# Optimization experiments

Measured on AMD Instinct MI355X. Metric: run time of the kernel, lower is better.

Reference implementation:

```python
import jax, jax.numpy as jnp
import numpy as np

B, L, D, H = 64, 1024, 256, 256


def setup_inputs() -> dict:
    key = jax.random.key(0)
    ks = jax.random.split(key, 10)
    s = 0.05  # small init to keep tanh/sigmoid in linear-ish range
    return {
        "x":  jax.random.normal(ks[0], (B, L, D), jnp.float32),
        # LSTM cell params (keras gate order i, f, g, o)
        "Wk": jax.random.normal(ks[1], (D, 4 * H), jnp.float32) * s,
        "Wr": jax.random.normal(ks[2], (H, 4 * H), jnp.float32) * s,
        "b":  jnp.zeros((4 * H,), jnp.float32),
        # Attention params
        "W1": jax.random.normal(ks[3], (D, H), jnp.float32) * s,
        "b1": jnp.zeros((H,), jnp.float32),
        "W2": jax.random.normal(ks[4], (H, H), jnp.float32) * s,
        "b2": jnp.zeros((H,), jnp.float32),
        "V":  jax.random.normal(ks[5], (H, 1), jnp.float32) * s,
        "bV": jnp.zeros((1,), jnp.float32),
    }


def reference(x, Wk, Wr, b, W1, b1, W2, b2, V, bV):
    Bb, Ll, Dd = x.shape
    Hh = Wr.shape[0]
    # Encoder projection, computed once (W1 @ encoder_outputs)
    w1_e = jnp.einsum('bld,dh->blh', x, W1) + b1            # (B, L, H)
    # Decoder input is the last encoder step, repeated every step
    x_in = x[:, -1, :]                                      # (B, D)
    xz = x_in @ Wk + b                                      # (B, 4H), constant per step
    h0 = jnp.zeros((Bb, Hh), x.dtype)
    c0 = jnp.zeros((Bb, Hh), x.dtype)

    def step(carry, _):
        h, c = carry
        z = xz + h @ Wr                                     # (B, 4H)
        i, f, g, o = jnp.split(z, 4, axis=-1)
        i = jax.nn.sigmoid(i)
        f = jax.nn.sigmoid(f)
        g = jnp.tanh(g)
        o = jax.nn.sigmoid(o)
        c = f * c + i * g
        h = o * jnp.tanh(c)
        # Additive (Bahdanau) attention: v^T tanh(W1 e + W2 d)
        w2_d = (h @ W2 + b2)[:, None, :]                    # (B, 1, H)
        scores = jnp.tanh(w1_e + w2_d) @ V + bV             # (B, L, 1)
        attn = jax.nn.softmax(scores[..., 0], axis=1)       # (B, L)
        return (h, c), attn

    _, attn_seq = jax.lax.scan(step, (h0, c0), None, length=Ll)  # (L, B, L)
    return jnp.transpose(attn_seq, (1, 0, 2))               # (B, L_steps, L_ptr)
```

## Files before the change

kernel.cpp:

```cpp
#include <hip/hip_runtime.h>
#include <hip/hip_bf16.h>


#define LOG2E  1.4426950408889634f
#define C2LOG2E 2.8853900817779268f

__device__ __forceinline__ unsigned f2bf(float f) {
  unsigned u = __builtin_bit_cast(unsigned, f);
  return (u + 0x7fffu + ((u >> 16) & 1u)) >> 16;
}
__device__ __forceinline__ float bfbits2f(unsigned bits) {
  return __builtin_bit_cast(float, bits << 16);
}

#if defined(__has_builtin)
#  if __has_builtin(__builtin_amdgcn_fdot2_f32_bf16)
#    define HAS_DOT2_BF16 1
#  endif
#endif

#if defined(HAS_DOT2_BF16)
typedef __bf16 bf16x2v __attribute__((ext_vector_type(2)));
__device__ __forceinline__ float dot2bf(unsigned w, unsigned h, float acc) {
  return __builtin_amdgcn_fdot2_f32_bf16(__builtin_bit_cast(bf16x2v, w),
                                         __builtin_bit_cast(bf16x2v, h), acc, false);
}
#else
__device__ __forceinline__ float dot2bf(unsigned w, unsigned h, float acc) {
  float wl = __builtin_bit_cast(float, w << 16);
  float wh = __builtin_bit_cast(float, w & 0xffff0000u);
  float hl = __builtin_bit_cast(float, h << 16);
  float hh = __builtin_bit_cast(float, h & 0xffff0000u);
  return fmaf(wh, hh, fmaf(wl, hl, acc));
}
#endif

#if defined(__has_builtin) && __has_builtin(__builtin_amdgcn_rcpf)
#  define FAST_RCP(x) __builtin_amdgcn_rcpf(x)
#else
#  define FAST_RCP(x) (1.0f / (x))
#endif

__device__ __forceinline__ float fast_sigmoid(float x) {
  return FAST_RCP(1.f + exp2f(-LOG2E * x));
}
__device__ __forceinline__ float fast_tanh(float x) {
  return 1.f - 2.f * FAST_RCP(1.f + exp2f(C2LOG2E * x));
}

__global__ __launch_bounds__(256) void k1_w1e(const float* __restrict__ x,
                                              const float* __restrict__ W1,
                                              const float* __restrict__ b1,
                                              unsigned short* __restrict__ AT) {
  const int b  = blockIdx.x >> 6;
  const int lb = blockIdx.x & 63;
  const int h  = threadIdx.x;
  float acc[16];
  const float bias = b1[h];
#pragma unroll
  for (int r = 0; r < 16; ++r) acc[r] = bias;
  const float* xb = x + ((size_t)(b * 1024 + lb * 16)) * 256;
  for (int d0 = 0; d0 < 256; d0 += 4) {
    const float w0 = W1[(d0 + 0) * 256 + h];
    const float w1 = W1[(d0 + 1) * 256 + h];
    const float w2 = W1[(d0 + 2) * 256 + h];
    const float w3 = W1[(d0 + 3) * 256 + h];
#pragma unroll
    for (int r = 0; r < 16; ++r) {
      const float4 xv = *(const float4*)(xb + r * 256 + d0);
      acc[r] = fmaf(xv.x, w0, acc[r]);
      acc[r] = fmaf(xv.y, w1, acc[r]);
      acc[r] = fmaf(xv.z, w2, acc[r]);
      acc[r] = fmaf(xv.w, w3, acc[r]);
    }
  }
  unsigned short* outp = AT + ((size_t)(b * 256 + h)) * 1024 + lb * 16;
#pragma unroll
  for (int r = 0; r < 16; r += 2) {
    unsigned u0 = f2bf(exp2f(C2LOG2E * acc[r]));
    unsigned u1 = f2bf(exp2f(C2LOG2E * acc[r + 1]));
    *(unsigned*)(outp + r) = u0 | (u1 << 16);
  }
}

__global__ __launch_bounds__(256) void k2_xz(const float* __restrict__ x,
                                             const float* __restrict__ Wk,
                                             const float* __restrict__ bvec,
                                             float* __restrict__ xz) {
  const int b = blockIdx.x, tid = threadIdx.x;
  float acc[4] = {bvec[tid], bvec[256 + tid], bvec[512 + tid], bvec[768 + tid]};
  const float* xr = x + ((size_t)b * 1024 + 1023) * 256;
  for (int d0 = 0; d0 < 256; d0 += 4) {
    const float4 xv = *(const float4*)(xr + d0);
#pragma unroll
    for (int i = 0; i < 4; ++i) {
      const float xs = (i == 0) ? xv.x : (i == 1) ? xv.y : (i == 2) ? xv.z : xv.w;
#pragma unroll
      for (int q = 0; q < 4; ++q)
        acc[q] = fmaf(xs, Wk[(size_t)(d0 + i) * 1024 + q * 256 + tid], acc[q]);
    }
  }
#pragma unroll
  for (int q = 0; q < 4; ++q) xz[b * 1024 + q * 256 + tid] = acc[q];
}

__global__ __launch_bounds__(512, 2) void k3_recur(const float* __restrict__ xz,
                                                   const float* __restrict__ Wr,
                                                   unsigned short* __restrict__ hseq) {
  __shared__ __align__(16) unsigned Wtail[8 * 1024 * 4];
  __shared__ float z_lds[512];
  __shared__ __align__(16) unsigned h_pk[128];
  const int b   = blockIdx.x;
  const int tid = threadIdx.x;
  const int colA = tid, colB = tid + 512;

  unsigned wA[96], wB[96];
#pragma unroll
  for (int p = 0; p < 96; ++p) {
    wA[p] = f2bf(Wr[(size_t)(2 * p) * 1024 + colA]) |
            (f2bf(Wr[(size_t)(2 * p + 1) * 1024 + colA]) << 16);
    wB[p] = f2bf(Wr[(size_t)(2 * p) * 1024 + colB]) |
            (f2bf(Wr[(size_t)(2 * p + 1) * 1024 + colB]) << 16);
  }
#pragma unroll
  for (int gg = 0; gg < 8; ++gg) {
#pragma unroll
    for (int d = 0; d < 4; ++d) {
      const int p = 96 + gg * 4 + d;
      Wtail[(gg * 1024 + colA) * 4 + d] =
          f2bf(Wr[(size_t)(2 * p) * 1024 + colA]) |
          (f2bf(Wr[(size_t)(2 * p + 1) * 1024 + colA]) << 16);
      Wtail[(gg * 1024 + colB) * 4 + d] =
          f2bf(Wr[(size_t)(2 * p) * 1024 + colB]) |
          (f2bf(Wr[(size_t)(2 * p + 1) * 1024 + colB]) << 16);
    }
  }
  if (tid < 128) h_pk[tid] = 0u;
  const float zaA = xz[b * 1024 + colA];
  const float zaB = xz[b * 1024 + colB];
  float c = 0.f;
  __syncthreads();

  for (int t = 0; t < 1024; ++t) {
    float aA = zaA, aB = zaB;
#pragma unroll
    for (int g = 0; g < 24; ++g) {
      const uint4 hp = *(const uint4*)&h_pk[4 * g];
      aA = dot2bf(wA[4 * g + 0], hp.x, aA);
      aA = dot2bf(wA[4 * g + 1], hp.y, aA);
      aA = dot2bf(wA[4 * g + 2], hp.z, aA);
      aA = dot2bf(wA[4 * g + 3], hp.w, aA);
      aB = dot2bf(wB[4 * g + 0], hp.x, aB);
      aB = dot2bf(wB[4 * g + 1], hp.y, aB);
      aB = dot2bf(wB[4 * g + 2], hp.z, aB);
      aB = dot2bf(wB[4 * g + 3], hp.w, aB);
    }
#pragma unroll
    for (int gg = 0; gg < 8; ++gg) {
      const uint4 hp = *(const uint4*)&h_pk[96 + 4 * gg];
      const uint4 wa = *(const uint4*)&Wtail[(gg * 1024 + colA) * 4];
      const uint4 wb = *(const uint4*)&Wtail[(gg * 1024 + colB) * 4];
      aA = dot2bf(wa.x, hp.x, aA);
      aA = dot2bf(wa.y, hp.y, aA);
      aA = dot2bf(wa.z, hp.z, aA);
      aA = dot2bf(wa.w, hp.w, aA);
      aB = dot2bf(wb.x, hp.x, aB);
      aB = dot2bf(wb.y, hp.y, aB);
      aB = dot2bf(wb.z, hp.z, aB);
      aB = dot2bf(wb.w, hp.w, aB);
    }
    if (tid >= 256) {
      z_lds[tid - 256] = aA;
      z_lds[tid]       = aB;
    }
    __syncthreads();
    if (tid < 256) {
      const float zi = aA;
      const float zg = aB;
      const float zf = z_lds[tid];
      const float zo = z_lds[tid + 256];
      const float ig = fast_sigmoid(zi);
      const float fg = fast_sigmoid(zf);
      const float gv = fast_tanh(zg);
      const float og = fast_sigmoid(zo);
      c = fmaf(fg, c, ig * gv);
      const float h = og * fast_tanh(c);
      const unsigned short hb = (unsigned short)f2bf(h);
      ((unsigned short*)h_pk)[tid] = hb;
      hseq[(size_t)(t * 64 + b) * 256 + tid] = hb;
    }
    __syncthreads();
  }
}

__global__ __launch_bounds__(256) void k3b_w2d(const unsigned int* __restrict__ hseq,
                                               const float* __restrict__ W2,
                                               const float* __restrict__ b2,
                                               float* __restrict__ D) {
  const int r0 = blockIdx.x * 16;
  const int h = threadIdx.x;
  float acc[16];
  const float bias = b2[h];
#pragma unroll
  for (int r = 0; r < 16; ++r) acc[r] = bias;
  for (int m0 = 0; m0 < 128; m0 += 2) {
    const float w0 = W2[(size_t)(2 * m0 + 0) * 256 + h];
    const float w1 = W2[(size_t)(2 * m0 + 1) * 256 + h];
    const float w2 = W2[(size_t)(2 * m0 + 2) * 256 + h];
    const float w3 = W2[(size_t)(2 * m0 + 3) * 256 + h];
#pragma unroll
    for (int r = 0; r < 16; ++r) {
      const uint2 hp = *(const uint2*)&hseq[(size_t)(r0 + r) * 128 + m0];
      acc[r] = fmaf(bfbits2f(hp.x),       w0, acc[r]);
      acc[r] = fmaf(bfbits2f(hp.x >> 16), w1, acc[r]);
      acc[r] = fmaf(bfbits2f(hp.y),       w2, acc[r]);
      acc[r] = fmaf(bfbits2f(hp.y >> 16), w3, acc[r]);
    }
  }
  const int t = r0 >> 6;
  const int bb0 = r0 & 63;
#pragma unroll
  for (int r = 0; r < 16; ++r) {
    D[((size_t)(bb0 + r) * 1024 + t) * 256 + h] = exp2f(C2LOG2E * acc[r]);
  }
}

__global__ __launch_bounds__(256) void k4_attn(const unsigned short* __restrict__ AT,
                                               const float* __restrict__ Dm,
                                               const float* __restrict__ V,
                                               float* __restrict__ out) {
  const int b  = blockIdx.x >> 6;
  const int tb = blockIdx.x & 63;
  const int wv = threadIdx.x >> 6;
  const int lane = threadIdx.x & 63;
  const int t0 = tb * 16 + wv * 4;
  const unsigned short* Ab = AT + (size_t)b * 256 * 1024;
  const float* Db = Dm + ((size_t)b * 1024 + t0) * 256;
  float acc[4][16];
#pragma unroll
  for (int tt = 0; tt < 4; ++tt)
#pragma unroll
    for (int lb = 0; lb < 16; ++lb) acc[tt][lb] = 0.f;

  for (int h = 0; h < 256; ++h) {
    const float vh = V[h];
    const float d0 = Db[h];
    const float d1 = Db[256 + h];
    const float d2 = Db[512 + h];
    const float d3 = Db[768 + h];
    const unsigned short* Ah = Ab + h * 1024 + lane;
#pragma unroll
    for (int lb = 0; lb < 16; ++lb) {
      const float a = bfbits2f((unsigned)Ah[lb * 64]);
      acc[0][lb] = fmaf(vh, FAST_RCP(fmaf(a, d0, 1.f)), acc[0][lb]);
      acc[1][lb] = fmaf(vh, FAST_RCP(fmaf(a, d1, 1.f)), acc[1][lb]);
      acc[2][lb] = fmaf(vh, FAST_RCP(fmaf(a, d2, 1.f)), acc[2][lb]);
      acc[3][lb] = fmaf(vh, FAST_RCP(fmaf(a, d3, 1.f)), acc[3][lb]);
    }
  }
#pragma unroll
  for (int tt = 0; tt < 4; ++tt) {
    float s[16];
    float m = -1e30f;
#pragma unroll
    for (int lb = 0; lb < 16; ++lb) {
      s[lb] = -2.f * acc[tt][lb];
      m = fmaxf(m, s[lb]);
    }
    for (int off = 32; off > 0; off >>= 1) m = fmaxf(m, __shfl_xor(m, off, 64));
    float p[16];
    float sum = 0.f;
#pragma unroll
    for (int lb = 0; lb < 16; ++lb) {
      p[lb] = exp2f((s[lb] - m) * LOG2E);
      sum += p[lb];
    }
    for (int off = 32; off > 0; off >>= 1) sum += __shfl_xor(sum, off, 64);
    const float rs = 1.f / sum;
    float* op = out + ((size_t)(b * 1024) + (t0 + tt)) * 1024 + lane;
#pragma unroll
    for (int lb = 0; lb < 16; ++lb) op[lb * 64] = p[lb] * rs;
  }
}

extern "C" void kernel_launch(void* const* d_in, const int* in_sizes, int n_in,
                              void* d_out, int out_size, void* d_ws, size_t ws_size,
                              hipStream_t stream) {
  (void)in_sizes; (void)n_in; (void)out_size; (void)ws_size;
  const float* x  = (const float*)d_in[0];
  const float* Wk = (const float*)d_in[1];
  const float* Wr = (const float*)d_in[2];
  const float* bb = (const float*)d_in[3];
  const float* W1 = (const float*)d_in[4];
  const float* b1 = (const float*)d_in[5];
  const float* W2 = (const float*)d_in[6];
  const float* b2 = (const float*)d_in[7];
  const float* V  = (const float*)d_in[8];

  char* ws = (char*)d_ws;
  float*          Dm   = (float*)(ws);
  unsigned short* AT   = (unsigned short*)(ws + 67108864);
  unsigned short* hseq = (unsigned short*)(ws + 100663296);
  float*          xz   = (float*)(ws + 134217728);
  float* out = (float*)d_out;

  hipLaunchKernelGGL(k1_w1e, dim3(4096), dim3(256), 0, stream, x, W1, b1, AT);
  hipLaunchKernelGGL(k2_xz, dim3(64), dim3(256), 0, stream, x, Wk, bb, xz);
  hipLaunchKernelGGL(k3_recur, dim3(64), dim3(512), 0, stream, xz, Wr, hseq);
  hipLaunchKernelGGL(k3b_w2d, dim3(4096), dim3(256), 0, stream, (const unsigned int*)hseq, W2, b2, Dm);
  hipLaunchKernelGGL(k4_attn, dim3(4096), dim3(256), 0, stream, AT, Dm, V, out);
}
```

Before: 4.266 ms.

## Combine four reciprocals into one and pack A in quads for attention

The attention kernel now sums four terms v_h/(1+a*d) over a common denominator, so it needs one fast reciprocal per four h values. It works on pairs of time steps with packed float2 math. To feed this, k1 rearranges the A tensor through shared memory so that four consecutive h values sit together as uint2 per position, letting k4 load them with one 8-byte access. The recurrent kernel also splits each dot-product chain into two accumulators to shorten the dependency chain. The trade is more multiplies and possible overflow or precision loss in the product of four denominators, plus an extra LDS transpose in k1.

```diff
diff --git a/kernel.cpp b/kernel.cpp
--- a/kernel.cpp
+++ b/kernel.cpp
@@ -4,6 +4,8 @@
 
 #define LOG2E  1.4426950408889634f
 #define C2LOG2E 2.8853900817779268f
+
+typedef float f32x2 __attribute__((ext_vector_type(2)));
 
 __device__ __forceinline__ unsigned f2bf(float f) {
   unsigned u = __builtin_bit_cast(unsigned, f);
@@ -11,6 +13,9 @@
 }
 __device__ __forceinline__ float bfbits2f(unsigned bits) {
   return __builtin_bit_cast(float, bits << 16);
+}
+__device__ __forceinline__ float bfhi2f(unsigned bits) {
+  return __builtin_bit_cast(float, bits & 0xffff0000u);
 }
 
 #if defined(__has_builtin)
@@ -51,7 +56,8 @@
 __global__ __launch_bounds__(256) void k1_w1e(const float* __restrict__ x,
                                               const float* __restrict__ W1,
                                               const float* __restrict__ b1,
-                                              unsigned short* __restrict__ AT) {
+                                              uint2* __restrict__ ATq) {
+  __shared__ unsigned short tile[256 * 16];
   const int b  = blockIdx.x >> 6;
   const int lb = blockIdx.x & 63;
   const int h  = threadIdx.x;
@@ -74,12 +80,22 @@
       acc[r] = fmaf(xv.w, w3, acc[r]);
     }
   }
-  unsigned short* outp = AT + ((size_t)(b * 256 + h)) * 1024 + lb * 16;
-#pragma unroll
-  for (int r = 0; r < 16; r += 2) {
-    unsigned u0 = f2bf(exp2f(C2LOG2E * acc[r]));
-    unsigned u1 = f2bf(exp2f(C2LOG2E * acc[r + 1]));
-    *(unsigned*)(outp + r) = u0 | (u1 << 16);
+#pragma unroll
+  for (int r = 0; r < 16; ++r)
+    tile[h * 16 + r] = (unsigned short)f2bf(exp2f(C2LOG2E * acc[r]));
+  __syncthreads();
+#pragma unroll
+  for (int k = 0; k < 4; ++k) {
+    const int o = k * 256 + threadIdx.x;
+    const int hq = o >> 4, lloc = o & 15;
+    const unsigned s0 = tile[(4 * hq + 0) * 16 + lloc];
+    const unsigned s1 = tile[(4 * hq + 1) * 16 + lloc];
+    const unsigned s2 = tile[(4 * hq + 2) * 16 + lloc];
+    const unsigned s3 = tile[(4 * hq + 3) * 16 + lloc];
+    uint2 val;
+    val.x = s0 | (s1 << 16);
+    val.y = s2 | (s3 << 16);
+    ATq[(((size_t)(b * 64 + hq)) << 10) + lb * 16 + lloc] = val;
   }
 }
 
@@ -142,33 +158,49 @@
   __syncthreads();
 
   for (int t = 0; t < 1024; ++t) {
-    float aA = zaA, aB = zaB;
-#pragma unroll
-    for (int g = 0; g < 24; ++g) {
+    float aA0 = zaA, aA1 = 0.f, aB0 = zaB, aB1 = 0.f;
+#pragma unroll
+    for (int g = 0; g < 12; ++g) {
       const uint4 hp = *(const uint4*)&h_pk[4 * g];
-      aA = dot2bf(wA[4 * g + 0], hp.x, aA);
-      aA = dot2bf(wA[4 * g + 1], hp.y, aA);
-      aA = dot2bf(wA[4 * g + 2], hp.z, aA);
-      aA = dot2bf(wA[4 * g + 3], hp.w, aA);
-      aB = dot2bf(wB[4 * g + 0], hp.x, aB);
-      aB = dot2bf(wB[4 * g + 1], hp.y, aB);
-      aB = dot2bf(wB[4 * g + 2], hp.z, aB);
-      aB = dot2bf(wB[4 * g + 3], hp.w, aB);
+      aA0 = dot2bf(wA[4 * g + 0], hp.x, aA0);
+      aA0 = dot2bf(wA[4 * g + 1], hp.y, aA0);
+      aA0 = dot2bf(wA[4 * g + 2], hp.z, aA0);
+      aA0 = dot2bf(wA[4 * g + 3], hp.w, aA0);
+      aB0 = dot2bf(wB[4 * g + 0], hp.x, aB0);
+      aB0 = dot2bf(wB[4 * g + 1], hp.y, aB0);
+      aB0 = dot2bf(wB[4 * g + 2], hp.z, aB0);
+      aB0 = dot2bf(wB[4 * g + 3], hp.w, aB0);
+    }
+#pragma unroll
+    for (int g = 12; g < 24; ++g) {
+      const uint4 hp = *(const uint4*)&h_pk[4 * g];
+      aA1 = dot2bf(wA[4 * g + 0], hp.x, aA1);
+      aA1 = dot2bf(wA[4 * g + 1], hp.y, aA1);
+      aA1 = dot2bf(wA[4 * g + 2], hp.z, aA1);
+      aA1 = dot2bf(wA[4 * g + 3], hp.w, aA1);
+      aB1 = dot2bf(wB[4 * g + 0], hp.x, aB1);
+      aB1 = dot2bf(wB[4 * g + 1], hp.y, aB1);
+      aB1 = dot2bf(wB[4 * g + 2], hp.z, aB1);
+      aB1 = dot2bf(wB[4 * g + 3], hp.w, aB1);
     }
 #pragma unroll
     for (int gg = 0; gg < 8; ++gg) {
       const uint4 hp = *(const uint4*)&h_pk[96 + 4 * gg];
       const uint4 wa = *(const uint4*)&Wtail[(gg * 1024 + colA) * 4];
       const uint4 wb = *(const uint4*)&Wtail[(gg * 1024 + colB) * 4];
-      aA = dot2bf(wa.x, hp.x, aA);
-      aA = dot2bf(wa.y, hp.y, aA);
-      aA = dot2bf(wa.z, hp.z, aA);
-      aA = dot2bf(wa.w, hp.w, aA);
-      aB = dot2bf(wb.x, hp.x, aB);
-      aB = dot2bf(wb.y, hp.y, aB);
-      aB = dot2bf(wb.z, hp.z, aB);
-      aB = dot2bf(wb.w, hp.w, aB);
-    }
+      float& rA = (gg < 4) ? aA0 : aA1;
+      float& rB = (gg < 4) ? aB0 : aB1;
+      rA = dot2bf(wa.x, hp.x, rA);
+      rA = dot2bf(wa.y, hp.y, rA);
+      rA = dot2bf(wa.z, hp.z, rA);
+      rA = dot2bf(wa.w, hp.w, rA);
+      rB = dot2bf(wb.x, hp.x, rB);
+      rB = dot2bf(wb.y, hp.y, rB);
+      rB = dot2bf(wb.z, hp.z, rB);
+      rB = dot2bf(wb.w, hp.w, rB);
+    }
+    const float aA = aA0 + aA1;
+    const float aB = aB0 + aB1;
     if (tid >= 256) {
       z_lds[tid - 256] = aA;
       z_lds[tid]       = aB;
@@ -225,62 +257,90 @@
   }
 }
 
-__global__ __launch_bounds__(256) void k4_attn(const unsigned short* __restrict__ AT,
-                                               const float* __restrict__ Dm,
-                                               const float* __restrict__ V,
-                                               float* __restrict__ out) {
+__global__ __launch_bounds__(256, 3) void k4_attn(const uint2* __restrict__ ATq,
+                                                  const float* __restrict__ Dm,
+                                                  const float* __restrict__ V,
+                                                  float* __restrict__ out) {
   const int b  = blockIdx.x >> 6;
   const int tb = blockIdx.x & 63;
   const int wv = threadIdx.x >> 6;
   const int lane = threadIdx.x & 63;
   const int t0 = tb * 16 + wv * 4;
-  const unsigned short* Ab = AT + (size_t)b * 256 * 1024;
-  const float* Db = Dm + ((size_t)b * 1024 + t0) * 256;
-  float acc[4][16];
-#pragma unroll
-  for (int tt = 0; tt < 4; ++tt)
-#pragma unroll
-    for (int lb = 0; lb < 16; ++lb) acc[tt][lb] = 0.f;
-
-  for (int h = 0; h < 256; ++h) {
-    const float vh = V[h];
-    const float d0 = Db[h];
-    const float d1 = Db[256 + h];
-    const float d2 = Db[512 + h];
-    const float d3 = Db[768 + h];
-    const unsigned short* Ah = Ab + h * 1024 + lane;
+  const uint2* Ab = ATq + (((size_t)b) << 16);
+  const float* Db = Dm + ((size_t)(b * 1024) + t0) * 256;
+  f32x2 acc2[2][16];
+#pragma unroll
+  for (int p = 0; p < 2; ++p)
+#pragma unroll
+    for (int lb = 0; lb < 16; ++lb) acc2[p][lb] = (f32x2){0.f, 0.f};
+
+  for (int hq = 0; hq < 64; ++hq) {
+    const float4 vq  = *(const float4*)(V + hq * 4);
+    const float4 Dr0 = *(const float4*)(Db + 0 * 256 + hq * 4);
+    const float4 Dr1 = *(const float4*)(Db + 1 * 256 + hq * 4);
+    const float4 Dr2 = *(const float4*)(Db + 2 * 256 + hq * 4);
+    const float4 Dr3 = *(const float4*)(Db + 3 * 256 + hq * 4);
+    f32x2 Dp[2][4];
+    Dp[0][0] = (f32x2){Dr0.x, Dr1.x}; Dp[0][1] = (f32x2){Dr0.y, Dr1.y};
+    Dp[0][2] = (f32x2){Dr0.z, Dr1.z}; Dp[0][3] = (f32x2){Dr0.w, Dr1.w};
+    Dp[1][0] = (f32x2){Dr2.x, Dr3.x}; Dp[1][1] = (f32x2){Dr2.y, Dr3.y};
+    Dp[1][2] = (f32x2){Dr2.z, Dr3.z}; Dp[1][3] = (f32x2){Dr2.w, Dr3.w};
+    const f32x2 v0 = (f32x2){vq.x, vq.x};
+    const f32x2 v1 = (f32x2){vq.y, vq.y};
+    const f32x2 v2 = (f32x2){vq.z, vq.z};
+    const f32x2 v3 = (f32x2){vq.w, vq.w};
+    const uint2* Ah = Ab + ((size_t)hq << 10) + lane;
 #pragma unroll
     for (int lb = 0; lb < 16; ++lb) {
-      const float a = bfbits2f((unsigned)Ah[lb * 64]);
-      acc[0][lb] = fmaf(vh, FAST_RCP(fmaf(a, d0, 1.f)), acc[0][lb]);
-      acc[1][lb] = fmaf(vh, FAST_RCP(fmaf(a, d1, 1.f)), acc[1][lb]);
-      acc[2][lb] = fmaf(vh, FAST_RCP(fmaf(a, d2, 1.f)), acc[2][lb]);
-      acc[3][lb] = fmaf(vh, FAST_RCP(fmaf(a, d3, 1.f)), acc[3][lb]);
-    }
-  }
-#pragma unroll
-  for (int tt = 0; tt < 4; ++tt) {
-    float s[16];
-    float m = -1e30f;
-#pragma unroll
-    for (int lb = 0; lb < 16; ++lb) {
-      s[lb] = -2.f * acc[tt][lb];
-      m = fmaxf(m, s[lb]);
-    }
-    for (int off = 32; off > 0; off >>= 1) m = fmaxf(m, __shfl_xor(m, off, 64));
-    float p[16];
-    float sum = 0.f;
-#pragma unroll
-    for (int lb = 0; lb < 16; ++lb) {
-      p[lb] = exp2f((s[lb] - m) * LOG2E);
-      sum += p[lb];
-    }
-    for (int off = 32; off > 0; off >>= 1) sum += __shfl_xor(sum, off, 64);
-    const float rs = 1.f / sum;
-    float* op = out + ((size_t)(b * 1024) + (t0 + tt)) * 1024 + lane;
-#pragma unroll
-    for (int lb = 0; lb < 16; ++lb) op[lb * 64] = p[lb] * rs;
-  }
+      const uint2 aq = Ah[lb * 64];
+      const f32x2 a0 = (f32x2){bfbits2f(aq.x), bfbits2f(aq.x)};
+      const f32x2 a1 = (f32x2){bfhi2f(aq.x),   bfhi2f(aq.x)};
+      const f32x2 a2 = (f32x2){bfbits2f(aq.y), bfbits2f(aq.y)};
+      const f32x2 a3 = (f32x2){bfhi2f(aq.y),   bfhi2f(aq.y)};
+      const f32x2 one = (f32x2){1.f, 1.f};
+#pragma unroll
+      for (int p = 0; p < 2; ++p) {
+        const f32x2 d0 = a0 * Dp[p][0] + one;
+        const f32x2 d1 = a1 * Dp[p][1] + one;
+        const f32x2 d2 = a2 * Dp[p][2] + one;
+        const f32x2 d3 = a3 * Dp[p][3] + one;
+        const f32x2 n01 = v0 * d1 + v1 * d0;
+        const f32x2 n23 = v2 * d3 + v3 * d2;
+        const f32x2 d01 = d0 * d1;
+        const f32x2 d23 = d2 * d3;
+        const f32x2 nf = n01 * d23 + n23 * d01;
+        const f32x2 df = d01 * d23;
+        const f32x2 r = (f32x2){FAST_RCP(df.x), FAST_RCP(df.y)};
+        acc2[p][lb] += nf * r;
+      }
+    }
+  }
+#pragma unroll
+  for (int p = 0; p < 2; ++p)
+#pragma unroll
+    for (int half = 0; half < 2; ++half) {
+      const int tt = 2 * p + half;
+      float s[16];
+      float m = -1e30f;
+#pragma unroll
+      for (int lb = 0; lb < 16; ++lb) {
+        s[lb] = -2.f * (half ? acc2[p][lb].y : acc2[p][lb].x);
+        m = fmaxf(m, s[lb]);
+      }
+      for (int off = 32; off > 0; off >>= 1) m = fmaxf(m, __shfl_xor(m, off, 64));
+      float pr[16];
+      float sum = 0.f;
+#pragma unroll
+      for (int lb = 0; lb < 16; ++lb) {
+        pr[lb] = exp2f((s[lb] - m) * LOG2E);
+        sum += pr[lb];
+      }
+      for (int off = 32; off > 0; off >>= 1) sum += __shfl_xor(sum, off, 64);
+      const float rs = 1.f / sum;
+      float* op = out + ((size_t)(b * 1024) + (t0 + tt)) * 1024 + lane;
+#pragma unroll
+      for (int lb = 0; lb < 16; ++lb) op[lb * 64] = pr[lb] * rs;
+    }
 }
 
 extern "C" void kernel_launch(void* const* d_in, const int* in_sizes, int n_in,
@@ -299,14 +359,14 @@
 
   char* ws = (char*)d_ws;
   float*          Dm   = (float*)(ws);
-  unsigned short* AT   = (unsigned short*)(ws + 67108864);
+  uint2*          ATq  = (uint2*)(ws + 67108864);
   unsigned short* hseq = (unsigned short*)(ws + 100663296);
   float*          xz   = (float*)(ws + 134217728);
   float* out = (float*)d_out;
 
-  hipLaunchKernelGGL(k1_w1e, dim3(4096), dim3(256), 0, stream, x, W1, b1, AT);
+  hipLaunchKernelGGL(k1_w1e, dim3(4096), dim3(256), 0, stream, x, W1, b1, ATq);
   hipLaunchKernelGGL(k2_xz, dim3(64), dim3(256), 0, stream, x, Wk, bb, xz);
   hipLaunchKernelGGL(k3_recur, dim3(64), dim3(512), 0, stream, xz, Wr, hseq);
   hipLaunchKernelGGL(k3b_w2d, dim3(4096), dim3(256), 0, stream, (const unsigned int*)hseq, W2, b2, Dm);
-  hipLaunchKernelGGL(k4_attn, dim3(4096), dim3(256), 0, stream, AT, Dm, V, out);
-}
+  hipLaunchKernelGGL(k4_attn, dim3(4096), dim3(256), 0, stream, ATq, Dm, V, out);
+}
```

Result: faster. 4.166 ms (-2.4%).
